# Optimization experiments

Hardware: AMD Instinct MI355X
Metric: run time of the kernel (lower is better)

Reference implementation:

```python
import jax, jax.numpy as jnp
import numpy as np

B, S, C, OUT = 8, 2048, 1024, 1024

def setup_inputs() -> dict:
    key = jax.random.key(0)
    ks = jax.random.split(key, 10)
    s = C ** -0.5
    return {
        "input": jax.random.normal(ks[0], (B, S, C), jnp.float32),
        "memory": jax.random.normal(ks[1], (B, S, C), jnp.float32),
        "Wq": jax.random.normal(ks[2], (C, C), jnp.float32) * s,
        "bq": jnp.zeros((C,), jnp.float32),
        "Wk": jax.random.normal(ks[3], (C, C), jnp.float32) * s,
        "bk": jnp.zeros((C,), jnp.float32),
        "Wv": jax.random.normal(ks[4], (C, C), jnp.float32) * s,
        "bv": jnp.zeros((C,), jnp.float32),
        "Wo": jax.random.normal(ks[5], (OUT, C), jnp.float32) * s,
        "bo": jnp.zeros((OUT,), jnp.float32),
    }

def reference(input, memory, Wq, bq, Wk, bk, Wv, bv, Wo, bo):
    depth_scale = input.shape[2] ** -0.5
    q = (input @ Wq.T + bq) * depth_scale          # [B, Sq, C]
    k = memory @ Wk.T + bk                          # [B, Sk, C]
    v = memory @ Wv.T + bv                          # [B, Sk, C]
    logit = jnp.einsum('bqc,bkc->bqk', q, k)        # [B, Sq, Sk]
    attn = jax.nn.softmax(logit, axis=-1)
    sel = jnp.einsum('bqk,bkc->bqc', attn, v)       # [B, Sq, C]
    return sel @ Wo.T + bo                          # [B, Sq, OUT]
```

## Files before the change

### kernel.cpp

```cpp
#include <hip/hip_runtime.h>
#include <hip/hip_bf16.h>


typedef __attribute__((ext_vector_type(8))) short short8;
typedef __attribute__((ext_vector_type(4))) float f32x4;

static __device__ __forceinline__ unsigned short f2bf(float f) {
  union { float f; unsigned u; } x; x.f = f;
  unsigned r = x.u + 0x7FFFu + ((x.u >> 16) & 1u);
  return (unsigned short)(r >> 16);
}

static __device__ __forceinline__ void g2l16(const void* g, void* l) {
  __builtin_amdgcn_global_load_lds(
      (const __attribute__((address_space(1))) void*)g,
      (__attribute__((address_space(3))) void*)l, 16, 0, 0);
}

template <int N> static __device__ __forceinline__ void vmw() {
  if constexpr (N == 4) asm volatile("s_waitcnt vmcnt(4)" ::: "memory");
  else                  asm volatile("s_waitcnt vmcnt(0)" ::: "memory");
}

static __device__ __forceinline__ long long brickoff(int r_, int k_, int Kd) {
  return (long long)(r_ >> 7) * ((long long)128 * Kd) +
         (long long)(k_ >> 5) * 4096 +
         (r_ & 127) * 32 +
         (((((k_ >> 3) & 3) ^ ((r_ >> 1) & 3))) << 3) +
         (k_ & 7);
}

__global__ __launch_bounds__(256) void cvt_brick_kernel(
    const float* __restrict__ s0, const float* __restrict__ s1,
    unsigned short* __restrict__ o0, unsigned short* __restrict__ o1,
    long long ngran) {
  const float* src = blockIdx.y ? s1 : s0;
  unsigned short* dst = blockIdx.y ? o1 : o0;
  long long gid = (long long)blockIdx.x * 256 + threadIdx.x;
  const long long stride = (long long)gridDim.x * 256;
  for (; gid < ngran; gid += stride) {
    const int tile = (int)(gid >> 14);
    const int g2 = (int)(gid & 16383);
    const int ks = g2 >> 9;
    const int rp = g2 & 511;
    const int r = rp >> 2;
    const int p = rp & 3;
    const int g = p ^ ((r >> 1) & 3);
    const float* sp = src + (long long)(tile * 128 + r) * 1024 + ks * 32 + g * 8;
    float4 u0 = ((const float4*)sp)[0];
    float4 u1 = ((const float4*)sp)[1];
    short8 pk;
    pk[0] = (short)f2bf(u0.x); pk[1] = (short)f2bf(u0.y);
    pk[2] = (short)f2bf(u0.z); pk[3] = (short)f2bf(u0.w);
    pk[4] = (short)f2bf(u1.x); pk[5] = (short)f2bf(u1.y);
    pk[6] = (short)f2bf(u1.z); pk[7] = (short)f2bf(u1.w);
    *(short8*)&dst[gid * 8] = pk;
  }
}

__global__ __launch_bounds__(256) void wcvt_brick_kernel(
    const float* __restrict__ w0, const float* __restrict__ w1,
    const float* __restrict__ w2, const float* __restrict__ w3,
    unsigned short* __restrict__ o0, unsigned short* __restrict__ o1,
    unsigned short* __restrict__ o2, unsigned short* __restrict__ o3) {
  const float* src; unsigned short* dst;
  switch (blockIdx.y) {
    case 0: src = w0; dst = o0; break;
    case 1: src = w1; dst = o1; break;
    case 2: src = w2; dst = o2; break;
    default: src = w3; dst = o3; break;
  }
  const int gid = blockIdx.x * 256 + threadIdx.x;
  const int tile = gid >> 14;
  const int g2 = gid & 16383;
  const int ks = g2 >> 9;
  const int rp = g2 & 511;
  const int r = rp >> 2;
  const int p = rp & 3;
  const int g = p ^ ((r >> 1) & 3);
  const float* sp = src + (long long)(tile * 128 + r) * 1024 + ks * 32 + g * 8;
  float4 u0 = ((const float4*)sp)[0];
  float4 u1 = ((const float4*)sp)[1];
  short8 pk;
  pk[0] = (short)f2bf(u0.x); pk[1] = (short)f2bf(u0.y);
  pk[2] = (short)f2bf(u0.z); pk[3] = (short)f2bf(u0.w);
  pk[4] = (short)f2bf(u1.x); pk[5] = (short)f2bf(u1.y);
  pk[6] = (short)f2bf(u1.z); pk[7] = (short)f2bf(u1.w);
  *(short8*)&dst[(long long)gid * 8] = pk;
}

#define EPI_BF16 0
#define EPI_BF16_TRANS 1
#define EPI_EXP 2
#define EPI_PV 3
#define EPI_F32 4

template <int EPI, bool HAS_BIAS>
__global__ __launch_bounds__(256, 3) void gemm_kernel(
    const unsigned short* __restrict__ A, const unsigned short* __restrict__ B,
    const float* __restrict__ bias, void* __restrict__ Dv,
    int NT, int ldaK, int ldbK, int ldd,
    long long sA, long long sBflat, int sBslice, int kOffB,
    long long sD, float scale) {
  constexpr int SL = 4096;

  int lin = blockIdx.x + gridDim.x * (blockIdx.y + gridDim.y * blockIdx.z);
  const int nwg = gridDim.x * gridDim.y * gridDim.z;
  lin = (lin & 7) * (nwg >> 3) + (lin >> 3);
  const int bx = lin % gridDim.x;
  int rem0 = lin / gridDim.x;
  const int by = rem0 % gridDim.y;
  const int bz = rem0 / gridDim.y;

  const int bm = bx * 128;
  const int bn = by * 128;
  const int tid = threadIdx.x;
  const int lane = tid & 63;
  const int wid = tid >> 6;
  const int wr = (wid >> 1) * 64;
  const int wc = (wid & 1) * 64;
  const int fr = lane & 15;
  const int hi = lane >> 4;
  const int rg = ((hi ^ ((fr >> 1) & 3)) << 3);

  __shared__ __align__(16) unsigned short As[3 * SL];
  __shared__ __align__(16) unsigned short Bs[3 * SL];

  f32x4 acc[4][4];
#pragma unroll
  for (int m = 0; m < 4; ++m)
#pragma unroll
    for (int n = 0; n < 4; ++n) acc[m][n] = (f32x4){0.f, 0.f, 0.f, 0.f};

  f32x4 asum[4];
  short8 ones;
#pragma unroll
  for (int m = 0; m < 4; ++m) asum[m] = (f32x4){0.f, 0.f, 0.f, 0.f};
#pragma unroll
  for (int j = 0; j < 8; ++j) ones[j] = (short)0x3F80;

  const unsigned short* Ab = A + bz * sA + (long long)(bm >> 7) * 128 * ldaK;
  const unsigned short* Bb = B + bz * sBflat + (long long)(bn >> 7) * 128 * ldbK +
                             (long long)(kOffB + bz * sBslice) * SL;
  auto stage = [&](int t, int buf) {
    const unsigned short* as = Ab + (long long)t * SL;
    const unsigned short* bs = Bb + (long long)t * SL;
#pragma unroll
    for (int i = 0; i < 2; ++i)
      g2l16(as + (i * 256 + tid) * 8, &As[buf * SL + (i * 256 + tid) * 8]);
#pragma unroll
    for (int i = 0; i < 2; ++i)
      g2l16(bs + (i * 256 + tid) * 8, &Bs[buf * SL + (i * 256 + tid) * 8]);
  };

  stage(0, 0);
  stage(1, 1);
  vmw<4>();
  __builtin_amdgcn_s_barrier();
  __builtin_amdgcn_sched_barrier(0);

  for (int t = 0; t < NT; ++t) {
    const int buf = t % 3;
    if (t + 2 < NT) stage(t + 2, (t + 2) % 3);

    short8 af[4], bf[4];
#pragma unroll
    for (int m = 0; m < 4; ++m)
      af[m] = *(const short8*)&As[buf * SL + (wr + m * 16 + fr) * 32 + rg];
#pragma unroll
    for (int n = 0; n < 4; ++n)
      bf[n] = *(const short8*)&Bs[buf * SL + (wc + n * 16 + fr) * 32 + rg];
    __builtin_amdgcn_s_setprio(1);
#pragma unroll
    for (int m = 0; m < 4; ++m)
#pragma unroll
      for (int n = 0; n < 4; ++n)
        acc[m][n] = __builtin_amdgcn_mfma_f32_16x16x32_bf16(af[m], bf[n],
                                                            acc[m][n], 0, 0, 0);
    if (EPI == EPI_PV) {
#pragma unroll
      for (int m = 0; m < 4; ++m)
        asum[m] = __builtin_amdgcn_mfma_f32_16x16x32_bf16(af[m], ones,
                                                          asum[m], 0, 0, 0);
    }
    __builtin_amdgcn_s_setprio(0);
    __builtin_amdgcn_sched_barrier(0);
    if (t + 2 < NT)      vmw<4>();
    else if (t + 1 < NT) vmw<0>();
    __builtin_amdgcn_s_barrier();
    __builtin_amdgcn_sched_barrier(0);
  }

  const int cr = hi * 4;
  const int cc = fr;
#pragma unroll
  for (int m = 0; m < 4; ++m) {
    const int row0 = bm + wr + m * 16 + cr;
#pragma unroll
    for (int n = 0; n < 4; ++n) {
      const int col = bn + wc + n * 16 + cc;
      const float bv = HAS_BIAS ? bias[col] : 0.f;
      if (EPI == EPI_F32) {
        float* D = (float*)Dv + bz * sD;
#pragma unroll
        for (int j = 0; j < 4; ++j)
          D[(long long)(row0 + j) * ldd + col] = acc[m][n][j] + bv;
      } else if (EPI == EPI_BF16) {
        unsigned short* D = (unsigned short*)Dv + bz * sD;
#pragma unroll
        for (int j = 0; j < 4; ++j)
          D[brickoff(row0 + j, col, ldd)] = f2bf((acc[m][n][j] + bv) * scale);
      } else if (EPI == EPI_BF16_TRANS) {
        unsigned short* D = (unsigned short*)Dv + bz * sD;
#pragma unroll
        for (int j = 0; j < 4; ++j)
          D[brickoff(col, row0 + j, ldd)] = f2bf((acc[m][n][j] + bv) * scale);
      } else if (EPI == EPI_EXP) {
        unsigned short* D = (unsigned short*)Dv + bz * sD;
#pragma unroll
        for (int j = 0; j < 4; ++j)
          D[brickoff(row0 + j, col, ldd)] = f2bf(__expf(acc[m][n][j]));
      } else {
        unsigned short* D = (unsigned short*)Dv + bz * sD;
#pragma unroll
        for (int j = 0; j < 4; ++j) {
          const float li = 1.f / asum[m][j];
          D[brickoff(row0 + j, col, ldd)] = f2bf(acc[m][n][j] * li);
        }
      }
    }
  }
}

extern "C" void kernel_launch(void* const* d_in, const int* in_sizes, int n_in,
                              void* d_out, int out_size, void* d_ws, size_t ws_size,
                              hipStream_t stream) {
  (void)in_sizes; (void)n_in; (void)out_size;
  const float* input  = (const float*)d_in[0];
  const float* memory = (const float*)d_in[1];
  const float* Wq = (const float*)d_in[2];
  const float* bq = (const float*)d_in[3];
  const float* Wk = (const float*)d_in[4];
  const float* bk = (const float*)d_in[5];
  const float* Wv = (const float*)d_in[6];
  const float* bv = (const float*)d_in[7];
  const float* Wo = (const float*)d_in[8];
  const float* bo = (const float*)d_in[9];
  float* out = (float*)d_out;

  const int S = 2048, C = 1024;
  const int CB = 4;
  const long long BS = 16384;
  const long long N_IN = BS * C;
  const long long N_W  = (long long)C * C;

  char* p = (char*)d_ws;
  auto alloc = [&](size_t bytes) {
    char* r = p;
    p += (bytes + 255) & ~(size_t)255;
    return r;
  };
  unsigned short* wqb  = (unsigned short*)alloc(N_W * 2);
  unsigned short* wkb  = (unsigned short*)alloc(N_W * 2);
  unsigned short* wvb  = (unsigned short*)alloc(N_W * 2);
  unsigned short* wob  = (unsigned short*)alloc(N_W * 2);
  unsigned short* Qb   = (unsigned short*)alloc(N_IN * 2);
  unsigned short* Kb   = (unsigned short*)alloc(N_IN * 2);
  unsigned short* Xb   = (unsigned short*)alloc(N_IN * 2);
  if ((size_t)(p - (char*)d_ws) > ws_size) return;

  unsigned short* Vt  = (unsigned short*)d_out;
  unsigned short* inb = (unsigned short*)d_out + N_IN;
  unsigned short* memb = Xb;
  unsigned short* Pt   = Xb;

  wcvt_brick_kernel<<<dim3(512, 4, 1), 256, 0, stream>>>(Wq, Wk, Wv, Wo,
                                                         wqb, wkb, wvb, wob);
  cvt_brick_kernel<<<dim3(2048, 2, 1), 256, 0, stream>>>(memory, input, memb, inb,
                                                         N_IN / 8);

  const float depth_scale = 0.03125f;

  gemm_kernel<EPI_BF16, true><<<dim3(128, 8, 1), 256, 0, stream>>>(
      memb, wkb, bk, Kb, 32, C, C, C, 0, 0, 0, 0, 0, 1.0f);
  gemm_kernel<EPI_BF16_TRANS, true><<<dim3(128, 8, 1), 256, 0, stream>>>(
      memb, wvb, bv, Vt, 32, C, C, (int)BS, 0, 0, 0, 0, 0, 1.0f);
  gemm_kernel<EPI_BF16, true><<<dim3(128, 8, 1), 256, 0, stream>>>(
      inb, wqb, bq, Qb, 32, C, C, C, 0, 0, 0, 0, 0, depth_scale);

  for (int c = 0; c < 8 / CB; ++c) {
    const long long qoff = (long long)c * CB * S * C;
    gemm_kernel<EPI_EXP, false><<<dim3(16, 16, CB), 256, 0, stream>>>(
        Qb + qoff, Kb + qoff, nullptr, Pt,
        32, C, C, S, (long long)S * C, (long long)S * C, 0, 0,
        (long long)S * S, 1.0f);
    gemm_kernel<EPI_PV, false><<<dim3(16, 8, CB), 256, 0, stream>>>(
        Pt, Vt, nullptr, Qb + qoff,
        64, S, (int)BS, C, (long long)S * S, 0, 64, c * CB * 64,
        (long long)S * C, 1.0f);
  }

  gemm_kernel<EPI_F32, true><<<dim3(128, 8, 1), 256, 0, stream>>>(
      Qb, wob, bo, out, 32, C, C, C, 0, 0, 0, 0, 0, 1.0f);
}
```

Before: 469.8 us.

## Load GEMM fragments directly from global into registers, dropping LDS staging

Removes the LDS triple-buffered global_load_lds staging and barriers from the GEMM kernel. Each wave now loads its MFMA fragments straight from the pre-swizzled brick layout in global memory into registers, double-buffered across K tiles. The tile rasterization order is also swapped so consecutive blocks walk the N dimension first. This drops LDS traffic and block synchronization, but A/B tiles are no longer shared across the waves of a block, which raises global/L2 traffic, and the odd-NT handling assumes NT is even.

```diff
diff --git a/kernel.cpp b/kernel.cpp
--- a/kernel.cpp
+++ b/kernel.cpp
@@ -9,17 +9,6 @@
   union { float f; unsigned u; } x; x.f = f;
   unsigned r = x.u + 0x7FFFu + ((x.u >> 16) & 1u);
   return (unsigned short)(r >> 16);
-}
-
-static __device__ __forceinline__ void g2l16(const void* g, void* l) {
-  __builtin_amdgcn_global_load_lds(
-      (const __attribute__((address_space(1))) void*)g,
-      (__attribute__((address_space(3))) void*)l, 16, 0, 0);
-}
-
-template <int N> static __device__ __forceinline__ void vmw() {
-  if constexpr (N == 4) asm volatile("s_waitcnt vmcnt(4)" ::: "memory");
-  else                  asm volatile("s_waitcnt vmcnt(0)" ::: "memory");
 }
 
 static __device__ __forceinline__ long long brickoff(int r_, int k_, int Kd) {
@@ -102,15 +91,13 @@
     int NT, int ldaK, int ldbK, int ldd,
     long long sA, long long sBflat, int sBslice, int kOffB,
     long long sD, float scale) {
-  constexpr int SL = 4096;
-
-  int lin = blockIdx.x + gridDim.x * (blockIdx.y + gridDim.y * blockIdx.z);
+  int i = blockIdx.x + gridDim.x * (blockIdx.y + gridDim.y * blockIdx.z);
   const int nwg = gridDim.x * gridDim.y * gridDim.z;
-  lin = (lin & 7) * (nwg >> 3) + (lin >> 3);
-  const int bx = lin % gridDim.x;
-  int rem0 = lin / gridDim.x;
-  const int by = rem0 % gridDim.y;
-  const int bz = rem0 / gridDim.y;
+  int v = (i & 7) * (nwg >> 3) + (i >> 3);
+  const int by = v % gridDim.y;
+  int u = v / gridDim.y;
+  const int bx = u % gridDim.x;
+  const int bz = u / gridDim.x;
 
   const int bm = bx * 128;
   const int bn = by * 128;
@@ -121,10 +108,7 @@
   const int wc = (wid & 1) * 64;
   const int fr = lane & 15;
   const int hi = lane >> 4;
-  const int rg = ((hi ^ ((fr >> 1) & 3)) << 3);
-
-  __shared__ __align__(16) unsigned short As[3 * SL];
-  __shared__ __align__(16) unsigned short Bs[3 * SL];
+  const int laneoff = fr * 32 + ((hi ^ ((fr >> 1) & 3)) << 3);
 
   f32x4 acc[4][4];
 #pragma unroll
@@ -139,57 +123,48 @@
 #pragma unroll
   for (int j = 0; j < 8; ++j) ones[j] = (short)0x3F80;
 
-  const unsigned short* Ab = A + bz * sA + (long long)(bm >> 7) * 128 * ldaK;
-  const unsigned short* Bb = B + bz * sBflat + (long long)(bn >> 7) * 128 * ldbK +
-                             (long long)(kOffB + bz * sBslice) * SL;
-  auto stage = [&](int t, int buf) {
-    const unsigned short* as = Ab + (long long)t * SL;
-    const unsigned short* bs = Bb + (long long)t * SL;
-#pragma unroll
-    for (int i = 0; i < 2; ++i)
-      g2l16(as + (i * 256 + tid) * 8, &As[buf * SL + (i * 256 + tid) * 8]);
-#pragma unroll
-    for (int i = 0; i < 2; ++i)
-      g2l16(bs + (i * 256 + tid) * 8, &Bs[buf * SL + (i * 256 + tid) * 8]);
-  };
-
-  stage(0, 0);
-  stage(1, 1);
-  vmw<4>();
-  __builtin_amdgcn_s_barrier();
-  __builtin_amdgcn_sched_barrier(0);
-
-  for (int t = 0; t < NT; ++t) {
-    const int buf = t % 3;
-    if (t + 2 < NT) stage(t + 2, (t + 2) % 3);
-
-    short8 af[4], bf[4];
+  const unsigned short* Ap = A + bz * sA + (long long)(bm >> 7) * 128 * ldaK +
+                             wr * 32 + laneoff;
+  const unsigned short* Bp = B + bz * sBflat + (long long)(bn >> 7) * 128 * ldbK +
+                             (long long)(kOffB + bz * sBslice) * 4096 +
+                             wc * 32 + laneoff;
+
+  short8 a0[4], b0[4], a1[4], b1[4];
+  auto LDA = [&](short8 (&d)[4], int t) {
+    const unsigned short* p = Ap + (long long)t * 4096;
+#pragma unroll
+    for (int m = 0; m < 4; ++m) d[m] = *(const short8*)(p + m * 512);
+  };
+  auto LDB = [&](short8 (&d)[4], int t) {
+    const unsigned short* p = Bp + (long long)t * 4096;
+#pragma unroll
+    for (int n = 0; n < 4; ++n) d[n] = *(const short8*)(p + n * 512);
+  };
+  auto FMA = [&](short8 (&a)[4], short8 (&b)[4]) {
 #pragma unroll
     for (int m = 0; m < 4; ++m)
-      af[m] = *(const short8*)&As[buf * SL + (wr + m * 16 + fr) * 32 + rg];
-#pragma unroll
-    for (int n = 0; n < 4; ++n)
-      bf[n] = *(const short8*)&Bs[buf * SL + (wc + n * 16 + fr) * 32 + rg];
-    __builtin_amdgcn_s_setprio(1);
-#pragma unroll
-    for (int m = 0; m < 4; ++m)
 #pragma unroll
       for (int n = 0; n < 4; ++n)
-        acc[m][n] = __builtin_amdgcn_mfma_f32_16x16x32_bf16(af[m], bf[n],
+        acc[m][n] = __builtin_amdgcn_mfma_f32_16x16x32_bf16(a[m], b[n],
                                                             acc[m][n], 0, 0, 0);
     if (EPI == EPI_PV) {
 #pragma unroll
       for (int m = 0; m < 4; ++m)
-        asum[m] = __builtin_amdgcn_mfma_f32_16x16x32_bf16(af[m], ones,
+        asum[m] = __builtin_amdgcn_mfma_f32_16x16x32_bf16(a[m], ones,
                                                           asum[m], 0, 0, 0);
     }
-    __builtin_amdgcn_s_setprio(0);
-    __builtin_amdgcn_sched_barrier(0);
-    if (t + 2 < NT)      vmw<4>();
-    else if (t + 1 < NT) vmw<0>();
-    __builtin_amdgcn_s_barrier();
-    __builtin_amdgcn_sched_barrier(0);
-  }
+  };
+
+  LDA(a0, 0); LDB(b0, 0);
+  LDA(a1, 1); LDB(b1, 1);
+  for (int t = 0; t < NT - 2; t += 2) {
+    FMA(a0, b0);
+    LDA(a0, t + 2); LDB(b0, t + 2);
+    FMA(a1, b1);
+    LDA(a1, t + 3); LDB(b1, t + 3);
+  }
+  FMA(a0, b0);
+  FMA(a1, b1);
 
   const int cr = hi * 4;
   const int cc = fr;
```

Result: faster. 396.0 us (-15.7%).
